# Performance work log

Hardware: AMD Instinct MI355X
Metric: run time of the kernel (lower is better)

The kernel has to match this reference:

```python
import jax, jax.numpy as jnp
import numpy as np

N = 100000      # nodes (single ntype)
R = 4           # edge types (relations)
E = 160000      # edges per relation
D_IN = 128
D_OUT = 128


def setup_inputs() -> dict:
    key = jax.random.key(0)
    k1, k2, k3, k4, k5 = jax.random.split(key, 5)
    gain = np.sqrt(2.0)  # calculate_gain('relu')
    bound = gain * np.sqrt(6.0 / (D_IN + D_OUT))  # xavier_uniform
    return {
        "x": jax.random.normal(k1, (N, D_IN), dtype=jnp.float32),
        "weight": jax.random.uniform(k2, (R, D_IN, D_OUT), dtype=jnp.float32,
                                     minval=-bound, maxval=bound),
        "loop_weight": jax.random.uniform(k3, (D_IN, D_OUT), dtype=jnp.float32,
                                          minval=-bound, maxval=bound),
        "h_bias": jnp.zeros((D_OUT,), dtype=jnp.float32),
        "src_idx": jax.random.randint(k4, (R, E), 0, N),
        "dst_idx": jax.random.randint(k5, (R, E), 0, N),
    }


def reference(x, weight, loop_weight, h_bias, src_idx, dst_idx):
    # Per-relation GraphConv(norm='right', weight external):
    #   h_r = segment_sum((x @ W_r)[src], dst) / clamp(in_degree, 1)
    # HeteroGraphConv default aggregation sums relations per dst node.
    n = x.shape[0]
    xw = jnp.einsum('nd,rdo->rno', x, weight)  # [R, N, D_OUT]
    h = jnp.zeros((n, weight.shape[2]), dtype=x.dtype)
    ones = jnp.ones((src_idx.shape[1],), dtype=x.dtype)
    for r in range(weight.shape[0]):  # small fixed relation count
        msg = xw[r][src_idx[r]]                                   # [E, D_OUT]
        agg = jax.ops.segment_sum(msg, dst_idx[r], num_segments=n)
        deg = jax.ops.segment_sum(ones, dst_idx[r], num_segments=n)
        h = h + agg / jnp.clip(deg, 1.0)[:, None]                 # norm='right'
    # self-loop + bias + activation (dropout=0 -> identity)
    h = h + x @ loop_weight + h_bias
    return jax.nn.relu(h)
```

## Files before the change

kernel.cpp:

```cpp
#include <hip/hip_runtime.h>

#define DD 128
#define KY 512
#define KT 640
#define RR 4
#define CAPL 4
#define CAP (1 << CAPL)

typedef short short8 __attribute__((ext_vector_type(8)));
typedef float f32x4 __attribute__((ext_vector_type(4)));

__device__ __forceinline__ unsigned short f2bf(float f) {
  unsigned u = __float_as_uint(f);
  u += 0x7fffu + ((u >> 16) & 1u);
  return (unsigned short)(u >> 16);
}

__global__ __launch_bounds__(256) void prep(const float* __restrict__ x,
                                            const float* __restrict__ weight,
                                            const float* __restrict__ loopw,
                                            const int* __restrict__ src,
                                            const int* __restrict__ dst,
                                            unsigned short* __restrict__ xb,
                                            unsigned short* __restrict__ wt,
                                            int* __restrict__ deg,
                                            int* __restrict__ slot,
                                            int N, int E, int XB, int WB) {
  int b = blockIdx.x;
  int t = threadIdx.x;
  if (b < XB) {
    int i = b * 256 + t;
    if (i >= (N + 1) * 16) return;
    int n = i >> 4;
    uint4 o = make_uint4(0, 0, 0, 0);
    if (n < N) {
      const float4* xp = (const float4*)x + (size_t)i * 2;
      float4 v0 = xp[0], v1 = xp[1];
      o.x = (unsigned)f2bf(v0.x) | ((unsigned)f2bf(v0.y) << 16);
      o.y = (unsigned)f2bf(v0.z) | ((unsigned)f2bf(v0.w) << 16);
      o.z = (unsigned)f2bf(v1.x) | ((unsigned)f2bf(v1.y) << 16);
      o.w = (unsigned)f2bf(v1.z) | ((unsigned)f2bf(v1.w) << 16);
    }
    ((uint4*)xb)[i] = o;
  } else if (b < XB + WB) {
    int i = (b - XB) * 256 + t;
    if (i >= DD * KT) return;
    int c = i / KT, k = i - c * KT;
    float v = (k < KY) ? weight[(size_t)(k >> 7) * DD * DD + (k & (DD - 1)) * DD + c]
                       : loopw[(size_t)(k - KY) * DD + c];
    wt[i] = f2bf(v);
  } else {
    int i = (b - XB - WB) * 256 + t;
    if (i >= RR * E) return;
    int r = i / E;
    size_t bk = (size_t)dst[i] * RR + r;
    int pos = atomicAdd(deg + bk, 1);
    if (pos < CAP) slot[(bk << CAPL) + pos] = src[i];
  }
}

__global__ __launch_bounds__(256) void gather_agg(const unsigned* __restrict__ xbu,
                                                  const int* __restrict__ slot,
                                                  const int* __restrict__ deg,
                                                  unsigned* __restrict__ yu,
                                                  int N) {
  int gid = blockIdx.x * 256 + threadIdx.x;
  int n = gid >> 6, lane = gid & 63;
  if (n >= N) return;

  int sv = slot[(size_t)n * 64 + lane];

  int4 dv = *(const int4*)(deg + (size_t)n * 4);
  int cn[RR], ct[RR];
  ct[0] = __builtin_amdgcn_readfirstlane(dv.x);
  ct[1] = __builtin_amdgcn_readfirstlane(dv.y);
  ct[2] = __builtin_amdgcn_readfirstlane(dv.z);
  ct[3] = __builtin_amdgcn_readfirstlane(dv.w);
#pragma unroll
  for (int r = 0; r < RR; r++) cn[r] = ct[r] > CAP ? CAP : ct[r];

  float ax[RR], ay[RR];
#pragma unroll
  for (int r = 0; r < RR; r++) { ax[r] = 0.f; ay[r] = 0.f; }

  int m = max(max(cn[0], cn[1]), max(cn[2], cn[3]));
  for (int i0 = 0; i0 < m; i0 += 4) {
    unsigned vv[4][RR];
#pragma unroll
    for (int u = 0; u < 4; u++) {
#pragma unroll
      for (int r = 0; r < RR; r++) {
        int i = i0 + u;
        int s = __builtin_amdgcn_readlane(sv, (r << 4) | (i & 15));
        s = (i < cn[r]) ? s : N;
        vv[u][r] = xbu[(size_t)s * 64 + lane];
      }
    }
#pragma unroll
    for (int u = 0; u < 4; u++)
#pragma unroll
      for (int r = 0; r < RR; r++) {
        ax[r] += __uint_as_float(vv[u][r] << 16);
        ay[r] += __uint_as_float(vv[u][r] & 0xffff0000u);
      }
  }
#pragma unroll
  for (int r = 0; r < RR; r++) {
    float inv = 1.0f / (float)max(ct[r], 1);
    yu[(size_t)n * (KY / 2) + r * 64 + lane] =
        (unsigned)f2bf(ax[r] * inv) | ((unsigned)f2bf(ay[r] * inv) << 16);
  }
}

#define LDA 40
__global__ __launch_bounds__(128) void gemm_mfma(const unsigned short* __restrict__ y,
                                                 const unsigned short* __restrict__ xb,
                                                 const unsigned short* __restrict__ wt,
                                                 const float* __restrict__ bias,
                                                 float* __restrict__ out, int N) {
  __shared__ unsigned short As[128 * LDA];
  __shared__ unsigned short Bs[128 * LDA];
  int t = threadIdx.x;
  int w = t >> 6, lane = t & 63;
  int row0 = blockIdx.x * 128;

  f32x4 acc[4][8];
#pragma unroll
  for (int i = 0; i < 4; i++)
#pragma unroll
    for (int c = 0; c < 8; c++) acc[i][c] = (f32x4){0.f, 0.f, 0.f, 0.f};

  for (int k0 = 0; k0 < KT; k0 += 32) {
    bool sely = (k0 < KY);
#pragma unroll
    for (int i = 0; i < 4; ++i) {
      int idx = t + i * 128;
      int row = idx >> 2;
      int seg = (idx & 3) * 8;
      int gr = row0 + row;
      uint4 va = make_uint4(0, 0, 0, 0);
      if (gr < N) {
        const unsigned short* ap =
            sely ? (y + (size_t)gr * KY + k0 + seg)
                 : (xb + (size_t)gr * DD + (k0 - KY) + seg);
        va = *(const uint4*)ap;
      }
      *(uint4*)(As + row * LDA + seg) = va;
      *(uint4*)(Bs + row * LDA + seg) = *(const uint4*)(wt + (size_t)row * KT + k0 + seg);
    }
    __syncthreads();
    int q8 = (lane >> 4) * 8;
    int m = lane & 15;
    short8 a[4], b[8];
#pragma unroll
    for (int i = 0; i < 4; ++i)
      a[i] = *(const short8*)(As + (w * 64 + i * 16 + m) * LDA + q8);
#pragma unroll
    for (int c = 0; c < 8; ++c)
      b[c] = *(const short8*)(Bs + (c * 16 + m) * LDA + q8);
#pragma unroll
    for (int i = 0; i < 4; ++i)
#pragma unroll
      for (int c = 0; c < 8; ++c)
        acc[i][c] = __builtin_amdgcn_mfma_f32_16x16x32_bf16(a[i], b[c], acc[i][c], 0, 0, 0);
    __syncthreads();
  }

  float bv[8];
#pragma unroll
  for (int c = 0; c < 8; ++c) bv[c] = bias[c * 16 + (lane & 15)];
#pragma unroll
  for (int i = 0; i < 4; ++i) {
    int rbase = row0 + w * 64 + i * 16 + (lane >> 4) * 4;
#pragma unroll
    for (int v = 0; v < 4; ++v) {
      int gr = rbase + v;
      if (gr < N) {
#pragma unroll
        for (int c = 0; c < 8; ++c)
          out[(size_t)gr * DD + c * 16 + (lane & 15)] = fmaxf(acc[i][c][v] + bv[c], 0.f);
      }
    }
  }
}

extern "C" void kernel_launch(void* const* d_in, const int* in_sizes, int n_in,
                              void* d_out, int out_size, void* d_ws, size_t ws_size,
                              hipStream_t stream) {
  const float* x      = (const float*)d_in[0];
  const float* weight = (const float*)d_in[1];
  const float* loop_w = (const float*)d_in[2];
  const float* h_bias = (const float*)d_in[3];
  const int*   src    = (const int*)d_in[4];
  const int*   dst    = (const int*)d_in[5];
  float* out = (float*)d_out;

  const int N = in_sizes[0] / DD;
  const int R = in_sizes[1] / (DD * DD);
  const int E = in_sizes[4] / R;
  const int RN = R * N, RE = R * E;

  char* p = (char*)d_ws;
  auto alloc = [&](size_t bytes) {
    char* q = p;
    p += (bytes + 63) & ~size_t(63);
    return q;
  };
  int* deg  = (int*)alloc((size_t)RN * 4);
  int* slot = (int*)alloc((size_t)RN * CAP * 4);
  unsigned short* wt = (unsigned short*)alloc((size_t)DD * KT * 2);
  unsigned short* xb = (unsigned short*)alloc((size_t)(N + 1) * DD * 2);
  unsigned short* y  = (unsigned short*)alloc((size_t)N * KY * 2);

  hipMemsetAsync(deg, 0, (size_t)RN * 4, stream);

  int XB = ((N + 1) * 16 + 255) / 256;
  int WB = (DD * KT + 255) / 256;
  int FB = (RE + 255) / 256;
  prep<<<XB + WB + FB, 256, 0, stream>>>(x, weight, loop_w, src, dst,
                                         xb, wt, deg, slot, N, E, XB, WB);
  gather_agg<<<((size_t)N * 64 + 255) / 256, 256, 0, stream>>>(
      (const unsigned*)xb, slot, deg, (unsigned*)y, N);
  gemm_mfma<<<(N + 127) / 128, 128, 0, stream>>>(y, xb, wt, h_bias, out, N);
}
```

Before: 269.8 us.

## Fuse neighbor gather-aggregation with MFMA GEMM via shared-memory tile

Merges the gather_agg and gemm_mfma kernels into one. Each 256-thread block aggregates 32 nodes into an LDS tile that also holds their self-loop features, then runs the bf16 MFMA GEMM against the weights read directly from global memory. This drops the write and re-read of the N×512 intermediate y buffer and one kernel launch. In exchange the GEMM tile shrinks to 32 rows per block, so B-operand reuse across rows is much lower. Weight fragments are now loaded from global or L2 on every k-step instead of being staged in shared memory.

```diff
diff --git a/kernel.cpp b/kernel.cpp
--- a/kernel.cpp
+++ b/kernel.cpp
@@ -6,6 +6,8 @@
 #define RR 4
 #define CAPL 4
 #define CAP (1 << CAPL)
+#define NPB 32
+#define LDA2 642
 
 typedef short short8 __attribute__((ext_vector_type(8)));
 typedef float f32x4 __attribute__((ext_vector_type(4)));
@@ -59,127 +61,102 @@
   }
 }
 
-__global__ __launch_bounds__(256) void gather_agg(const unsigned* __restrict__ xbu,
-                                                  const int* __restrict__ slot,
-                                                  const int* __restrict__ deg,
-                                                  unsigned* __restrict__ yu,
-                                                  int N) {
-  int gid = blockIdx.x * 256 + threadIdx.x;
-  int n = gid >> 6, lane = gid & 63;
-  if (n >= N) return;
-
-  int sv = slot[(size_t)n * 64 + lane];
-
-  int4 dv = *(const int4*)(deg + (size_t)n * 4);
-  int cn[RR], ct[RR];
-  ct[0] = __builtin_amdgcn_readfirstlane(dv.x);
-  ct[1] = __builtin_amdgcn_readfirstlane(dv.y);
-  ct[2] = __builtin_amdgcn_readfirstlane(dv.z);
-  ct[3] = __builtin_amdgcn_readfirstlane(dv.w);
-#pragma unroll
-  for (int r = 0; r < RR; r++) cn[r] = ct[r] > CAP ? CAP : ct[r];
-
-  float ax[RR], ay[RR];
-#pragma unroll
-  for (int r = 0; r < RR; r++) { ax[r] = 0.f; ay[r] = 0.f; }
-
-  int m = max(max(cn[0], cn[1]), max(cn[2], cn[3]));
-  for (int i0 = 0; i0 < m; i0 += 4) {
-    unsigned vv[4][RR];
-#pragma unroll
-    for (int u = 0; u < 4; u++) {
-#pragma unroll
-      for (int r = 0; r < RR; r++) {
-        int i = i0 + u;
-        int s = __builtin_amdgcn_readlane(sv, (r << 4) | (i & 15));
-        s = (i < cn[r]) ? s : N;
-        vv[u][r] = xbu[(size_t)s * 64 + lane];
-      }
-    }
-#pragma unroll
-    for (int u = 0; u < 4; u++)
-#pragma unroll
-      for (int r = 0; r < RR; r++) {
-        ax[r] += __uint_as_float(vv[u][r] << 16);
-        ay[r] += __uint_as_float(vv[u][r] & 0xffff0000u);
-      }
-  }
-#pragma unroll
-  for (int r = 0; r < RR; r++) {
-    float inv = 1.0f / (float)max(ct[r], 1);
-    yu[(size_t)n * (KY / 2) + r * 64 + lane] =
-        (unsigned)f2bf(ax[r] * inv) | ((unsigned)f2bf(ay[r] * inv) << 16);
-  }
-}
-
-#define LDA 40
-__global__ __launch_bounds__(128) void gemm_mfma(const unsigned short* __restrict__ y,
-                                                 const unsigned short* __restrict__ xb,
-                                                 const unsigned short* __restrict__ wt,
-                                                 const float* __restrict__ bias,
-                                                 float* __restrict__ out, int N) {
-  __shared__ unsigned short As[128 * LDA];
-  __shared__ unsigned short Bs[128 * LDA];
+__global__ __launch_bounds__(256) void gather_gemm(
+    const unsigned* __restrict__ xbu,
+    const int* __restrict__ slot,
+    const int* __restrict__ deg,
+    const unsigned short* __restrict__ wt,
+    const float* __restrict__ bias,
+    float* __restrict__ out, int N) {
+  __shared__ unsigned short As[NPB * LDA2];
+  unsigned* Asu = (unsigned*)As;
   int t = threadIdx.x;
   int w = t >> 6, lane = t & 63;
-  int row0 = blockIdx.x * 128;
-
-  f32x4 acc[4][8];
-#pragma unroll
-  for (int i = 0; i < 4; i++)
-#pragma unroll
-    for (int c = 0; c < 8; c++) acc[i][c] = (f32x4){0.f, 0.f, 0.f, 0.f};
+  int nb = blockIdx.x * NPB;
+
+  for (int j = 0; j < NPB / 4; ++j) {
+    int nl = w * (NPB / 4) + j;
+    int n = nb + nl;
+    unsigned arow = (unsigned)nl * (LDA2 / 2);
+    if (n < N) {
+      int sv = slot[(size_t)n * 64 + lane];
+      int4 dv = *(const int4*)(deg + (size_t)n * 4);
+      int ct[RR], cn[RR];
+      ct[0] = __builtin_amdgcn_readfirstlane(dv.x);
+      ct[1] = __builtin_amdgcn_readfirstlane(dv.y);
+      ct[2] = __builtin_amdgcn_readfirstlane(dv.z);
+      ct[3] = __builtin_amdgcn_readfirstlane(dv.w);
+#pragma unroll
+      for (int r = 0; r < RR; r++) cn[r] = ct[r] > CAP ? CAP : ct[r];
+
+      float ax[RR], ay[RR];
+#pragma unroll
+      for (int r = 0; r < RR; r++) { ax[r] = 0.f; ay[r] = 0.f; }
+
+      int m = max(max(cn[0], cn[1]), max(cn[2], cn[3]));
+      for (int i0 = 0; i0 < m; i0 += 4) {
+        unsigned vv[4][RR];
+#pragma unroll
+        for (int u = 0; u < 4; u++) {
+#pragma unroll
+          for (int r = 0; r < RR; r++) {
+            int i = i0 + u;
+            int s = __builtin_amdgcn_readlane(sv, (r << 4) | (i & 15));
+            s = (i < cn[r]) ? s : N;
+            vv[u][r] = xbu[(size_t)s * 64 + lane];
+          }
+        }
+#pragma unroll
+        for (int u = 0; u < 4; u++)
+#pragma unroll
+          for (int r = 0; r < RR; r++) {
+            ax[r] += __uint_as_float(vv[u][r] << 16);
+            ay[r] += __uint_as_float(vv[u][r] & 0xffff0000u);
+          }
+      }
+#pragma unroll
+      for (int r = 0; r < RR; r++) {
+        float inv = 1.0f / (float)max(ct[r], 1);
+        Asu[arow + r * 64 + lane] =
+            (unsigned)f2bf(ax[r] * inv) | ((unsigned)f2bf(ay[r] * inv) << 16);
+      }
+      Asu[arow + 256 + lane] = xbu[(size_t)n * 64 + lane];
+    } else {
+#pragma unroll
+      for (int r = 0; r < RR + 1; r++) Asu[arow + r * 64 + lane] = 0u;
+    }
+  }
+
+  __syncthreads();
+
+  int m = lane & 15;
+  int q8 = (lane >> 4) * 8;
+  int mt = w & 1;
+  int cb = (w >> 1) * 64;
+
+  f32x4 acc4[4];
+#pragma unroll
+  for (int c = 0; c < 4; c++) acc4[c] = (f32x4){0.f, 0.f, 0.f, 0.f};
 
   for (int k0 = 0; k0 < KT; k0 += 32) {
-    bool sely = (k0 < KY);
-#pragma unroll
-    for (int i = 0; i < 4; ++i) {
-      int idx = t + i * 128;
-      int row = idx >> 2;
-      int seg = (idx & 3) * 8;
-      int gr = row0 + row;
-      uint4 va = make_uint4(0, 0, 0, 0);
-      if (gr < N) {
-        const unsigned short* ap =
-            sely ? (y + (size_t)gr * KY + k0 + seg)
-                 : (xb + (size_t)gr * DD + (k0 - KY) + seg);
-        va = *(const uint4*)ap;
-      }
-      *(uint4*)(As + row * LDA + seg) = va;
-      *(uint4*)(Bs + row * LDA + seg) = *(const uint4*)(wt + (size_t)row * KT + k0 + seg);
-    }
-    __syncthreads();
-    int q8 = (lane >> 4) * 8;
-    int m = lane & 15;
-    short8 a[4], b[8];
-#pragma unroll
-    for (int i = 0; i < 4; ++i)
-      a[i] = *(const short8*)(As + (w * 64 + i * 16 + m) * LDA + q8);
-#pragma unroll
-    for (int c = 0; c < 8; ++c)
-      b[c] = *(const short8*)(Bs + (c * 16 + m) * LDA + q8);
-#pragma unroll
-    for (int i = 0; i < 4; ++i)
-#pragma unroll
-      for (int c = 0; c < 8; ++c)
-        acc[i][c] = __builtin_amdgcn_mfma_f32_16x16x32_bf16(a[i], b[c], acc[i][c], 0, 0, 0);
-    __syncthreads();
-  }
-
-  float bv[8];
-#pragma unroll
-  for (int c = 0; c < 8; ++c) bv[c] = bias[c * 16 + (lane & 15)];
-#pragma unroll
-  for (int i = 0; i < 4; ++i) {
-    int rbase = row0 + w * 64 + i * 16 + (lane >> 4) * 4;
-#pragma unroll
-    for (int v = 0; v < 4; ++v) {
-      int gr = rbase + v;
-      if (gr < N) {
-#pragma unroll
-        for (int c = 0; c < 8; ++c)
-          out[(size_t)gr * DD + c * 16 + (lane & 15)] = fmaxf(acc[i][c][v] + bv[c], 0.f);
-      }
+    short8 a = *(const short8*)(As + (mt * 16 + m) * LDA2 + k0 + q8);
+#pragma unroll
+    for (int c = 0; c < 4; c++) {
+      short8 b = *(const short8*)(wt + (size_t)(cb + c * 16 + m) * KT + k0 + q8);
+      acc4[c] = __builtin_amdgcn_mfma_f32_16x16x32_bf16(a, b, acc4[c], 0, 0, 0);
+    }
+  }
+
+  float bv[4];
+#pragma unroll
+  for (int c = 0; c < 4; c++) bv[c] = bias[cb + c * 16 + m];
+#pragma unroll
+  for (int v = 0; v < 4; v++) {
+    int gr = nb + mt * 16 + (lane >> 4) * 4 + v;
+    if (gr < N) {
+#pragma unroll
+      for (int c = 0; c < 4; c++)
+        out[(size_t)gr * DD + cb + c * 16 + m] = fmaxf(acc4[c][v] + bv[c], 0.f);
     }
   }
 }
@@ -210,7 +187,6 @@
   int* slot = (int*)alloc((size_t)RN * CAP * 4);
   unsigned short* wt = (unsigned short*)alloc((size_t)DD * KT * 2);
   unsigned short* xb = (unsigned short*)alloc((size_t)(N + 1) * DD * 2);
-  unsigned short* y  = (unsigned short*)alloc((size_t)N * KY * 2);
 
   hipMemsetAsync(deg, 0, (size_t)RN * 4, stream);
 
@@ -219,7 +195,6 @@
   int FB = (RE + 255) / 256;
   prep<<<XB + WB + FB, 256, 0, stream>>>(x, weight, loop_w, src, dst,
                                          xb, wt, deg, slot, N, E, XB, WB);
-  gather_agg<<<((size_t)N * 64 + 255) / 256, 256, 0, stream>>>(
-      (const unsigned*)xb, slot, deg, (unsigned*)y, N);
-  gemm_mfma<<<(N + 127) / 128, 128, 0, stream>>>(y, xb, wt, h_bias, out, N);
-}
+  gather_gemm<<<(N + NPB - 1) / NPB, 256, 0, stream>>>(
+      (const unsigned*)xb, slot, deg, wt, h_bias, out, N);
+}
```

Result: slower. 318.9 us (+18.2%).
